# Performance work log

Measured on AMD Instinct MI355X. Metric: run time of the kernel, lower is better.

## Reference

```python
import jax, jax.numpy as jnp
import numpy as np


def setup_inputs() -> dict:
    key = jax.random.key(0)
    k1, k2, k3, k4 = jax.random.split(key, 4)
    n_smps, n_fcns, d_in, d_out = 16384, 2048, 32, 32
    GAIN = 1e-5  # xavier gain used by init_wts / init_offsets
    x = jax.random.normal(k1, (n_smps, d_in), dtype=jnp.float32)
    ctrs = jax.random.normal(k2, (n_fcns, d_in), dtype=jnp.float32)
    wts = jax.random.normal(k3, (n_fcns, d_in, d_out), dtype=jnp.float32) * GAIN
    offsets = jax.random.normal(k4, (n_fcns, d_out), dtype=jnp.float32) * GAIN
    return {"x": x, "ctrs": ctrs, "wts": wts, "offsets": offsets, "k": 4}


def reference(x, ctrs, wts, offsets, k):
    # --- knn_do equivalent (done under no_grad in torch) ---
    # squared Euclidean distance: (n_smps, n_fcns)
    x_sg = jax.lax.stop_gradient(x)
    c_sg = jax.lax.stop_gradient(ctrs)
    d2 = (jnp.sum(x_sg * x_sg, axis=1, keepdims=True)
          - 2.0 * (x_sg @ c_sg.T)
          + jnp.sum(c_sg * c_sg, axis=1)[None, :])
    _, idx = jax.lax.top_k(-d2, k)  # (n_smps, k), nearest centers

    # --- gather per-neighbor local linear models ---
    sel_wts = wts[idx]        # (n_smps, k, d_in, d_out)
    sel_ctrs = ctrs[idx]      # (n_smps, k, d_in)
    sel_offs = offsets[idx]   # (n_smps, k, d_out)

    applied_wts = jnp.sum(sel_wts, axis=1)  # (n_smps, d_in, d_out)
    # offsets minus sum over neighbors/d_in of wts * ctrs
    applied_offsets = (jnp.sum(sel_offs, axis=1)
                       - jnp.einsum('nkde,nkd->ne', sel_wts, sel_ctrs))
    # y = x @ applied_wts + applied_offsets, per sample
    y = jnp.einsum('nde,nd->ne', applied_wts, x) + applied_offsets
    return y
```

## Files before the change

### kernel.cpp

```cpp
#include <hip/hip_runtime.h>
#include <math.h>

typedef short bf16x8 __attribute__((ext_vector_type(8)));
typedef float f32x4  __attribute__((ext_vector_type(4)));

#define N_SMPS 16384
#define N_FCNS 2048
#define D_IN 32
#define D_OUT 32
#define KNN 4
#define SPLITS 4
#define CPS 512
#define TILES 32
#define POOL 48
#define SMP 16

__device__ __forceinline__ unsigned umin_u(unsigned a, unsigned b) { return a < b ? a : b; }
__device__ __forceinline__ unsigned umax_u(unsigned a, unsigned b) { return a > b ? a : b; }

__device__ __forceinline__ unsigned short bf16_rne(float f) {
  unsigned b = __float_as_uint(f);
  unsigned r = b + 0x7FFFu + ((b >> 16) & 1u);
  return (unsigned short)(r >> 16);
}

#define OFF_CH   0u
#define OFF_HB   131072u

#define NC4 (N_FCNS * D_IN / 4)

__global__ __launch_bounds__(256) void k_prep(
    const float* __restrict__ ctrs,
    unsigned short* __restrict__ ch, float* __restrict__ hb)
{
  const int gt = blockIdx.x * 256 + threadIdx.x;
  float4 v = ((const float4*)ctrs)[gt];
  ushort4 o;
  o.x = bf16_rne(v.x); o.y = bf16_rne(v.y);
  o.z = bf16_rne(v.z); o.w = bf16_rne(v.w);
  ((ushort4*)ch)[gt] = o;

  if (gt < N_FCNS) {
    const float4* cp4 = (const float4*)(ctrs + (size_t)gt * D_IN);
    float a = 0.f;
    #pragma unroll
    for (int q = 0; q < 8; ++q) {
      float4 c = cp4[q];
      a += c.x * c.x + c.y * c.y + c.z * c.z + c.w * c.w;
    }
    hb[gt] = -0.5f * a;
  }
}

__global__ __launch_bounds__(256) void k_mega(
    const unsigned short* __restrict__ ch,
    const float* __restrict__ hb,
    const float* __restrict__ x, const float* __restrict__ ctrs,
    const float* __restrict__ wts, const float* __restrict__ offs,
    float* __restrict__ y)
{
  __shared__ __align__(16) char u_mem[16640];
  __shared__ float    s_hb[SPLITS * CPS];
  __shared__ unsigned s_pool[SMP][POOL];
  __shared__ double   s_pd2[SMP][POOL];
  __shared__ int      s_pix[SMP][POOL];
  __shared__ int      s_sel[SMP][KNN];
  __shared__ __align__(16) unsigned short s_xh[SMP * D_IN];

  unsigned* s_cand = (unsigned*)u_mem;
  float*    s_diff = (float*)u_mem;
  float4*   s_part = (float4*)(u_mem + 8448);

  const int tid = threadIdx.x;
  const int lane = tid & 63;
  const int w = __builtin_amdgcn_readfirstlane(tid >> 6);
  const int col = lane & 15;
  const int quad = lane >> 4;
  const int sbase = blockIdx.x * SMP;
  const int nbase0 = w * CPS;

  #pragma unroll
  for (int r = 0; r < CPS / 64; ++r)
    s_hb[nbase0 + r * 64 + lane] = hb[nbase0 + r * 64 + lane];

  if (tid < 128) {
    const int s = tid >> 3;
    const int q = tid & 7;
    float4 v = ((const float4*)(x + (size_t)(sbase + s) * D_IN))[q];
    ushort4 o;
    o.x = bf16_rne(v.x); o.y = bf16_rne(v.y);
    o.z = bf16_rne(v.z); o.w = bf16_rne(v.w);
    ((ushort4*)s_xh)[tid] = o;
  }

  __syncthreads();

  const bf16x8 ah = *(const bf16x8*)(s_xh + col * D_IN + quad * 8);

  unsigned ls[4][4];
  #pragma unroll
  for (int r = 0; r < 4; ++r)
    #pragma unroll
    for (int e = 0; e < 4; ++e) ls[r][e] = 0u;

  const unsigned short* chb =
      ch + (size_t)nbase0 * D_IN + (size_t)col * D_IN + quad * 8;
  #define BLOAD(t) (*(const bf16x8*)(chb + (size_t)(t) * 16 * D_IN))
  #define HLOAD(t) (s_hb[nbase0 + (t) * 16 + col])

  bf16x8 bh[4];
  float  hv[4];
  #pragma unroll
  for (int p = 0; p < 4; ++p) { bh[p] = BLOAD(p); hv[p] = HLOAD(p); }

  for (int t = 0; t < TILES; t += 4) {
    #pragma unroll
    for (int p = 0; p < 4; ++p) {
      {
        f32x4 acc = {0.f, 0.f, 0.f, 0.f};
        acc = __builtin_amdgcn_mfma_f32_16x16x32_bf16(ah, bh[p], acc, 0, 0, 0);
        const unsigned tc = (unsigned)((t + p) * 16 + col);
        const float hvv = hv[p];
        #pragma unroll
        for (int r = 0; r < 4; ++r) {
          const float uu = acc[r] + hvv;
          unsigned b = __float_as_uint(uu);
          unsigned m = b ^ ((unsigned)((int)b >> 31) | 0x80000000u);
          unsigned key = (m & 0xFFFFFE00u) | tc;
          unsigned t0 = umin_u(ls[r][0], key); ls[r][0] = umax_u(ls[r][0], key);
          unsigned t1 = umin_u(ls[r][1], t0);  ls[r][1] = umax_u(ls[r][1], t0);
          unsigned t2 = umin_u(ls[r][2], t1);  ls[r][2] = umax_u(ls[r][2], t1);
          ls[r][3] = umax_u(ls[r][3], t2);
        }
      }
      const int tn = (t + 4 + p) & (TILES - 1);
      bh[p] = BLOAD(tn);
      hv[p] = HLOAD(tn);
    }
  }
  #undef BLOAD
  #undef HLOAD

  #pragma unroll
  for (int r = 0; r < 4; ++r) {
    const int row = quad * 4 + r;
    *(uint4*)&s_cand[(((w * 16) + row) * 16 + col) * 4] =
        make_uint4(ls[r][0], ls[r][1], ls[r][2], ls[r][3]);
  }
  __syncthreads();

  if (tid < 128) {
    const int sl = tid >> 3;
    const int g  = tid & 7;
    const int wv = g >> 1;
    const int chh = (g & 1) * 8;
    unsigned q0 = 0, q1 = 0, q2 = 0, q3 = 0, q4 = 0, q5 = 0;
    #pragma unroll
    for (int c2 = 0; c2 < 8; ++c2) {
      uint4 kv = *(const uint4*)&s_cand[(((wv * 16) + sl) * 16 + chh + c2) * 4];
      unsigned ks[4] = {kv.x, kv.y, kv.z, kv.w};
      #pragma unroll
      for (int e = 0; e < 4; ++e) {
        unsigned key = ks[e];
        unsigned t0 = umin_u(q0, key); q0 = umax_u(q0, key);
        unsigned t1 = umin_u(q1, t0);  q1 = umax_u(q1, t0);
        unsigned t2 = umin_u(q2, t1);  q2 = umax_u(q2, t1);
        unsigned t3 = umin_u(q3, t2);  q3 = umax_u(q3, t2);
        unsigned t4 = umin_u(q4, t3);  q4 = umax_u(q4, t3);
        q5 = umax_u(q5, t4);
      }
    }
    unsigned* op = &s_pool[sl][g * 6];
    op[0] = q0; op[1] = q1; op[2] = q2;
    op[3] = q3; op[4] = q4; op[5] = q5;
  }
  __syncthreads();

  for (int c = tid; c < SMP * POOL; c += 256) {
    const int sl = c / POOL;
    const int p = c - sl * POOL;
    const unsigned key = s_pool[sl][p];
    const int wv = p / 12;
    const int j = wv * CPS + (int)(key & 0x1FFu);
    const float4* xp4 = (const float4*)(x + (size_t)(sbase + sl) * D_IN);
    const float4* cp4 = (const float4*)(ctrs + (size_t)j * D_IN);
    double d2a = 0.0, d2b = 0.0;
    #pragma unroll
    for (int q = 0; q < 8; ++q) {
      float4 cv = cp4[q];
      float4 xv = xp4[q];
      double df0 = (double)xv.x - (double)cv.x;
      double df1 = (double)xv.y - (double)cv.y;
      double df2 = (double)xv.z - (double)cv.z;
      double df3 = (double)xv.w - (double)cv.w;
      d2a = fma(df0, df0, d2a);
      d2b = fma(df1, df1, d2b);
      d2a = fma(df2, df2, d2a);
      d2b = fma(df3, df3, d2b);
    }
    s_pd2[sl][p] = d2a + d2b;
    s_pix[sl][p] = j;
  }
  __syncthreads();

  if (tid < SMP) {
    double bd[4]; int b4[4];
    #pragma unroll
    for (int e = 0; e < 4; ++e) { bd[e] = 1e300; b4[e] = 0x7fffffff; }
    for (int m = 0; m < POOL; ++m) {
      const double d2 = s_pd2[tid][m];
      const int j = s_pix[tid][m];
      bool ins = (d2 < bd[3]) || (d2 == bd[3] && j < b4[3]);
      if (ins) {
        bd[3] = d2; b4[3] = j;
        #pragma unroll
        for (int q = 3; q > 0; --q) {
          bool sw = (bd[q] < bd[q - 1]) ||
                    (bd[q] == bd[q - 1] && b4[q] < b4[q - 1]);
          if (sw) {
            double td = bd[q]; bd[q] = bd[q - 1]; bd[q - 1] = td;
            int    tj = b4[q]; b4[q] = b4[q - 1]; b4[q - 1] = tj;
          }
        }
      }
    }
    #pragma unroll
    for (int q = 0; q < 4; ++q) s_sel[tid][q] = b4[q];
  }
  __syncthreads();

  #pragma unroll
  for (int r = 0; r < SMP * KNN * D_IN / 256; ++r) {
    int v = r * 256 + tid;
    int d = v & 31; int p = v >> 5;
    int sl = p >> 2; int j = p & 3;
    int f = s_sel[sl][j];
    s_diff[(sl * KNN + j) * (D_IN + 1) + d] =
        x[(size_t)(sbase + sl) * D_IN + d] - ctrs[(size_t)f * D_IN + d];
  }
  __syncthreads();

  #pragma unroll
  for (int r = 0; r < 2; ++r) {
    const int slot = r * 256 + tid;
    const int sl = slot >> 5;
    const int j  = (slot >> 3) & 3;
    const int eq = slot & 7;
    const int f = s_sel[sl][j];
    const float4* wp = (const float4*)(wts + (size_t)f * (D_IN * D_OUT));
    float4 acc = ((const float4*)(offs + (size_t)f * D_OUT))[eq];
    #pragma unroll
    for (int d = 0; d < D_IN; ++d) {
      float4 wv = wp[d * 8 + eq];
      float xc = s_diff[(sl * KNN + j) * (D_IN + 1) + d];
      acc.x = fmaf(xc, wv.x, acc.x);
      acc.y = fmaf(xc, wv.y, acc.y);
      acc.z = fmaf(xc, wv.z, acc.z);
      acc.w = fmaf(xc, wv.w, acc.w);
    }
    s_part[(sl * KNN + j) * 8 + eq] = acc;
  }
  __syncthreads();

  #pragma unroll
  for (int r = 0; r < 2; ++r) {
    const int slot = r * 256 + tid;
    const int sl = slot >> 5;
    const int j  = (slot >> 3) & 3;
    const int eq = slot & 7;
    if (j == 0) {
      float4 a = s_part[(sl * KNN + 0) * 8 + eq];
      float4 b = s_part[(sl * KNN + 1) * 8 + eq];
      float4 c = s_part[(sl * KNN + 2) * 8 + eq];
      float4 e = s_part[(sl * KNN + 3) * 8 + eq];
      float4 o;
      o.x = (a.x + b.x) + (c.x + e.x);
      o.y = (a.y + b.y) + (c.y + e.y);
      o.z = (a.z + b.z) + (c.z + e.z);
      o.w = (a.w + b.w) + (c.w + e.w);
      ((float4*)(y + (size_t)(sbase + sl) * D_OUT))[eq] = o;
    }
  }
}

extern "C" void kernel_launch(void* const* d_in, const int* in_sizes, int n_in,
                              void* d_out, int out_size, void* d_ws, size_t ws_size,
                              hipStream_t stream) {
  const float* x    = (const float*)d_in[0];
  const float* ctrs = (const float*)d_in[1];
  const float* wts  = (const float*)d_in[2];
  const float* offs = (const float*)d_in[3];
  float* y = (float*)d_out;

  char* ws = (char*)d_ws;
  unsigned short* ch = (unsigned short*)(ws + OFF_CH);
  float*          hb = (float*)(ws + OFF_HB);

  k_prep<<<NC4 / 256, 256, 0, stream>>>(ctrs, ch, hb);
  k_mega<<<N_SMPS / SMP, 256, 0, stream>>>(ch, hb, x, ctrs, wts, offs, y);
}
```

Measured before the change: 120.9 us.

## Store weights as bf16 in prep, alias pool buffers into union, swizzle candidate LDS

The prep kernel now also converts the full weight tensor to bf16 in workspace. The main kernel reads these halved-size weights and expands them to fp32 in registers, cutting gather bandwidth for the per-neighbor linear models. The distance pool arrays move into the shared union buffer with a padded stride, and the candidate scratch uses an XOR swizzle to reduce LDS bank conflicts and shared memory use. The cost is an extra 8 MB read and 4 MB write per call in prep, plus reduced weight precision in the output.

```diff
diff --git a/kernel.cpp b/kernel.cpp
--- a/kernel.cpp
+++ b/kernel.cpp
@@ -13,6 +13,7 @@
 #define CPS 512
 #define TILES 32
 #define POOL 48
+#define PPOOL 49
 #define SMP 16
 
 __device__ __forceinline__ unsigned umin_u(unsigned a, unsigned b) { return a < b ? a : b; }
@@ -26,19 +27,26 @@
 
 #define OFF_CH   0u
 #define OFF_HB   131072u
+#define OFF_WB   (OFF_HB + 8192u)
 
 #define NC4 (N_FCNS * D_IN / 4)
+#define NW4 (N_FCNS * D_IN * D_OUT / 4)
+#define NTOT (NC4 + NW4)
 
 __global__ __launch_bounds__(256) void k_prep(
-    const float* __restrict__ ctrs,
-    unsigned short* __restrict__ ch, float* __restrict__ hb)
+    const float* __restrict__ ctrs, const float* __restrict__ wts,
+    unsigned short* __restrict__ ch, unsigned short* __restrict__ wb,
+    float* __restrict__ hb)
 {
   const int gt = blockIdx.x * 256 + threadIdx.x;
-  float4 v = ((const float4*)ctrs)[gt];
+  const float* src; unsigned short* dst; int i4;
+  if (gt < NC4) { src = ctrs; dst = ch; i4 = gt; }
+  else          { src = wts;  dst = wb; i4 = gt - NC4; }
+  float4 v = ((const float4*)src)[i4];
   ushort4 o;
   o.x = bf16_rne(v.x); o.y = bf16_rne(v.y);
   o.z = bf16_rne(v.z); o.w = bf16_rne(v.w);
-  ((ushort4*)ch)[gt] = o;
+  ((ushort4*)dst)[i4] = o;
 
   if (gt < N_FCNS) {
     const float4* cp4 = (const float4*)(ctrs + (size_t)gt * D_IN);
@@ -56,18 +64,18 @@
     const unsigned short* __restrict__ ch,
     const float* __restrict__ hb,
     const float* __restrict__ x, const float* __restrict__ ctrs,
-    const float* __restrict__ wts, const float* __restrict__ offs,
+    const unsigned short* __restrict__ wb, const float* __restrict__ offs,
     float* __restrict__ y)
 {
   __shared__ __align__(16) char u_mem[16640];
   __shared__ float    s_hb[SPLITS * CPS];
   __shared__ unsigned s_pool[SMP][POOL];
-  __shared__ double   s_pd2[SMP][POOL];
-  __shared__ int      s_pix[SMP][POOL];
   __shared__ int      s_sel[SMP][KNN];
   __shared__ __align__(16) unsigned short s_xh[SMP * D_IN];
 
   unsigned* s_cand = (unsigned*)u_mem;
+  double*   s_pd2  = (double*)u_mem;
+  int*      s_pix  = (int*)(u_mem + 6272);
   float*    s_diff = (float*)u_mem;
   float4*   s_part = (float4*)(u_mem + 8448);
 
@@ -144,7 +152,7 @@
   #pragma unroll
   for (int r = 0; r < 4; ++r) {
     const int row = quad * 4 + r;
-    *(uint4*)&s_cand[(((w * 16) + row) * 16 + col) * 4] =
+    *(uint4*)&s_cand[(((w * 16) + row) * 16 + (col ^ row)) * 4] =
         make_uint4(ls[r][0], ls[r][1], ls[r][2], ls[r][3]);
   }
   __syncthreads();
@@ -157,7 +165,8 @@
     unsigned q0 = 0, q1 = 0, q2 = 0, q3 = 0, q4 = 0, q5 = 0;
     #pragma unroll
     for (int c2 = 0; c2 < 8; ++c2) {
-      uint4 kv = *(const uint4*)&s_cand[(((wv * 16) + sl) * 16 + chh + c2) * 4];
+      uint4 kv = *(const uint4*)
+          &s_cand[(((wv * 16) + sl) * 16 + ((chh + c2) ^ sl)) * 4];
       unsigned ks[4] = {kv.x, kv.y, kv.z, kv.w};
       #pragma unroll
       for (int e = 0; e < 4; ++e) {
@@ -198,8 +207,8 @@
       d2a = fma(df2, df2, d2a);
       d2b = fma(df3, df3, d2b);
     }
-    s_pd2[sl][p] = d2a + d2b;
-    s_pix[sl][p] = j;
+    s_pd2[sl * PPOOL + p] = d2a + d2b;
+    s_pix[sl * PPOOL + p] = j;
   }
   __syncthreads();
 
@@ -208,8 +217,8 @@
     #pragma unroll
     for (int e = 0; e < 4; ++e) { bd[e] = 1e300; b4[e] = 0x7fffffff; }
     for (int m = 0; m < POOL; ++m) {
-      const double d2 = s_pd2[tid][m];
-      const int j = s_pix[tid][m];
+      const double d2 = s_pd2[tid * PPOOL + m];
+      const int j = s_pix[tid * PPOOL + m];
       bool ins = (d2 < bd[3]) || (d2 == bd[3] && j < b4[3]);
       if (ins) {
         bd[3] = d2; b4[3] = j;
@@ -247,16 +256,20 @@
     const int j  = (slot >> 3) & 3;
     const int eq = slot & 7;
     const int f = s_sel[sl][j];
-    const float4* wp = (const float4*)(wts + (size_t)f * (D_IN * D_OUT));
+    const uint2* wp = (const uint2*)(wb + (size_t)f * (D_IN * D_OUT));
     float4 acc = ((const float4*)(offs + (size_t)f * D_OUT))[eq];
     #pragma unroll
     for (int d = 0; d < D_IN; ++d) {
-      float4 wv = wp[d * 8 + eq];
+      uint2 wv = wp[d * 8 + eq];
+      float w0 = __uint_as_float(wv.x << 16);
+      float w1 = __uint_as_float(wv.x & 0xFFFF0000u);
+      float w2 = __uint_as_float(wv.y << 16);
+      float w3 = __uint_as_float(wv.y & 0xFFFF0000u);
       float xc = s_diff[(sl * KNN + j) * (D_IN + 1) + d];
-      acc.x = fmaf(xc, wv.x, acc.x);
-      acc.y = fmaf(xc, wv.y, acc.y);
-      acc.z = fmaf(xc, wv.z, acc.z);
-      acc.w = fmaf(xc, wv.w, acc.w);
+      acc.x = fmaf(xc, w0, acc.x);
+      acc.y = fmaf(xc, w1, acc.y);
+      acc.z = fmaf(xc, w2, acc.z);
+      acc.w = fmaf(xc, w3, acc.w);
     }
     s_part[(sl * KNN + j) * 8 + eq] = acc;
   }
@@ -295,7 +308,8 @@
   char* ws = (char*)d_ws;
   unsigned short* ch = (unsigned short*)(ws + OFF_CH);
   float*          hb = (float*)(ws + OFF_HB);
-
-  k_prep<<<NC4 / 256, 256, 0, stream>>>(ctrs, ch, hb);
-  k_mega<<<N_SMPS / SMP, 256, 0, stream>>>(ch, hb, x, ctrs, wts, offs, y);
+  unsigned short* wb = (unsigned short*)(ws + OFF_WB);
+
+  k_prep<<<NTOT / 256, 256, 0, stream>>>(ctrs, wts, ch, wb, hb);
+  k_mega<<<N_SMPS / SMP, 256, 0, stream>>>(ch, hb, x, ctrs, wb, offs, y);
 }
```

New measurement: 111.0 us. -8.2%, faster.
